# Optimization experiments

Measured on AMD Instinct MI355X. Metric: run time of the kernel, lower is better.

Reference implementation:

```python
import jax, jax.numpy as jnp
import numpy as np

H = 4      # num_heads
F = 64     # node_in_feats
FE = 16    # edge_in_feats
N = 4096   # num_nodes
E = 65536  # num_edges (avg degree 16)


def setup_inputs() -> dict:
    key = jax.random.key(0)
    ks = jax.random.split(key, 6)
    return {
        "node_inputs": jax.random.normal(ks[0], (N, F), jnp.float32),
        "edge_inputs": jax.random.normal(ks[1], (E, FE), jnp.float32),
        "src": jax.random.randint(ks[2], (E,), 0, N, jnp.int32),
        "dst": jax.random.randint(ks[3], (E,), 0, N, jnp.int32),
        "Wn": jax.random.normal(ks[4], (F, F * H), jnp.float32) / np.sqrt(F).astype(np.float32),
        "bn": jnp.zeros((F * H,), jnp.float32),
        "We": jax.random.normal(ks[5], (FE, H), jnp.float32) / np.sqrt(FE).astype(np.float32),
        "be": jnp.zeros((H,), jnp.float32),
    }


def reference(node_inputs, edge_inputs, src, dst, Wn, bn, We, be):
    # node linear projection: [N, H*F] then torch .view(H, -1, F) == row-major reshape
    node_proj = (node_inputs @ Wn + bn).reshape(H, N, F)
    # edge linear projection: [E, H] then torch .view(H, -1, 1) == row-major reshape
    edge_proj = (edge_inputs @ We + be).reshape(H, E)
    # self-attention: scale by sqrt(edge_in_feats), softmax over dim=1 (all edges per head)
    attn = jax.nn.softmax(edge_proj / np.float32(np.sqrt(FE)), axis=1)  # [H, E]
    # dense attention projection: projection[h, src[e], dst[e]] = attn[h, e]
    proj = jnp.zeros((H, N, N), jnp.float32).at[:, src, dst].set(attn)  # [H, N, N]
    # message passing ('sum' aggregation): proj @ node_proj -> [H, N, F]
    msg = jnp.einsum('hsd,hdf->hsf', proj, node_proj)
    # head pooling 'mean' over head dim (-3)
    return msg.mean(axis=0)  # [N, F]
```

## Files before the change

kernel.cpp:

```cpp
#include <hip/hip_runtime.h>

#define TBL_BITS 18
#define TBL_SIZE (1u << TBL_BITS)
#define TBL_MASK (TBL_SIZE - 1u)

#define GBLK 1024
#define BLK  256


struct Args {
    const float* X;  const float* Xe;
    const int* src;  const int* dst;
    const float* Wn; const float* bn;
    const float* We; const float* be;
    float* out;
    float* nproj;
    float* ep;
    float* partials;
    float* stats;
    unsigned long long* tbl;
};

__device__ __forceinline__ unsigned hash_key(unsigned key) {
    return (key * 2654435761u) >> (32 - TBL_BITS);
}

__global__ __launch_bounds__(BLK, 4) void k_p0(Args A) {
    const int tid = blockIdx.x * BLK + threadIdx.x;
    {
        const float4 z = make_float4(0.f, 0.f, 0.f, 0.f);
        if (tid < 65536)       ((float4*)A.out)[tid] = z;
        else if (tid < 196608) ((float4*)A.tbl)[tid - 65536] = z;
    }
    if (tid < 131072) {
        const int c = tid & 255;
        const int g = tid >> 8;
        const float b = A.bn[c];
        float acc[8];
#pragma unroll
        for (int r = 0; r < 8; ++r) acc[r] = b;
        const float* Wc = A.Wn + c;
#pragma unroll 8
        for (int k = 0; k < 64; ++k) {
            const float w = Wc[k * 256];
#pragma unroll
            for (int r = 0; r < 8; ++r)
                acc[r] = fmaf(A.X[(g + 512 * r) * 64 + k], w, acc[r]);
        }
#pragma unroll
        for (int r = 0; r < 8; ++r)
            A.nproj[(g + 512 * r) * 256 + c] = acc[r];
    }
    if (tid < 65536) {
        const float4* xi = (const float4*)(A.Xe + (size_t)tid * 16);
        float x[16];
        float4 v;
        v = xi[0]; x[0]=v.x;  x[1]=v.y;  x[2]=v.z;  x[3]=v.w;
        v = xi[1]; x[4]=v.x;  x[5]=v.y;  x[6]=v.z;  x[7]=v.w;
        v = xi[2]; x[8]=v.x;  x[9]=v.y;  x[10]=v.z; x[11]=v.w;
        v = xi[3]; x[12]=v.x; x[13]=v.y; x[14]=v.z; x[15]=v.w;
        float a0 = A.be[0], a1 = A.be[1], a2 = A.be[2], a3 = A.be[3];
#pragma unroll
        for (int k = 0; k < 16; ++k) {
            a0 = fmaf(x[k], A.We[k * 4 + 0], a0);
            a1 = fmaf(x[k], A.We[k * 4 + 1], a1);
            a2 = fmaf(x[k], A.We[k * 4 + 2], a2);
            a3 = fmaf(x[k], A.We[k * 4 + 3], a3);
        }
        const float e0 = expf(a0 * 0.25f), e1 = expf(a1 * 0.25f);
        const float e2 = expf(a2 * 0.25f), e3 = expf(a3 * 0.25f);
        ((float4*)A.ep)[tid] = make_float4(e0, e1, e2, e3);
        float s = e0 + e1 + e2 + e3;
#pragma unroll
        for (int off = 32; off > 0; off >>= 1) s += __shfl_xor(s, off);
        if ((tid & 63) == 0) A.partials[tid >> 6] = s;
    }
}

__global__ __launch_bounds__(BLK, 4) void k_p1(Args A) {
    const int tid = blockIdx.x * BLK + threadIdx.x;
    {
        const unsigned key = ((unsigned)A.src[tid] << 12) | (unsigned)A.dst[tid];
        const unsigned long long tag  = (unsigned long long)(key + 1u);
        const unsigned long long pack = (tag << 24) | (unsigned long long)tid;
        unsigned i = hash_key(key);
        while (true) {
            unsigned long long cur = A.tbl[i];
            if (cur == 0ull) {
                unsigned long long old = atomicCAS(&A.tbl[i], 0ull, pack);
                if (old == 0ull) break;
                cur = old;
            }
            if ((cur >> 24) == tag) {
                atomicMax(&A.tbl[i], pack);
                break;
            }
            i = (i + 1u) & TBL_MASK;
        }
    }
    if (blockIdx.x == 0) {
        __shared__ float4 red[256];
        const int t = threadIdx.x;
        red[t] = make_float4(A.partials[t], A.partials[256 + t],
                             A.partials[512 + t], A.partials[768 + t]);
        __syncthreads();
        for (int s = 128; s > 0; s >>= 1) {
            if (t < s) {
                red[t].x += red[t + s].x; red[t].y += red[t + s].y;
                red[t].z += red[t + s].z; red[t].w += red[t + s].w;
            }
            __syncthreads();
        }
        if (t == 0) {
            A.stats[0] = 0.25f / red[0].x;
            A.stats[1] = 0.25f / red[0].y;
            A.stats[2] = 0.25f / red[0].z;
            A.stats[3] = 0.25f / red[0].w;
        }
    }
}

__global__ __launch_bounds__(BLK, 4) void k_p2(Args A) {
    const int tid = blockIdx.x * BLK + threadIdx.x;
    const int w = tid >> 6;
    const int f = tid & 63;
    const float r0 = A.stats[0], r1 = A.stats[1];
    const float r2 = A.stats[2], r3 = A.stats[3];
#pragma unroll
    for (int i = 0; i < 8; i += 4) {
        int e[4], s[4], d[4];
        unsigned long long tag[4], cur[4];
        unsigned idx[4];
#pragma unroll
        for (int j = 0; j < 4; ++j) {
            e[j] = w * 8 + i + j;
            s[j] = A.src[e[j]];
            d[j] = A.dst[e[j]];
            const unsigned key = ((unsigned)s[j] << 12) | (unsigned)d[j];
            tag[j] = (unsigned long long)(key + 1u);
            idx[j] = hash_key(key);
        }
#pragma unroll
        for (int j = 0; j < 4; ++j) cur[j] = A.tbl[idx[j]];
#pragma unroll
        for (int j = 0; j < 4; ++j)
            while ((cur[j] >> 24) != tag[j]) {
                idx[j] = (idx[j] + 1u) & TBL_MASK;
                cur[j] = A.tbl[idx[j]];
            }
#pragma unroll
        for (int j = 0; j < 4; ++j) {
            if ((unsigned)(cur[j] & 0xFFFFFFull) != (unsigned)e[j]) continue;
            const float a0 = A.ep[e[j]];
            const float a1 = A.ep[65536 + e[j]];
            const float a2 = A.ep[131072 + e[j]];
            const float a3 = A.ep[196608 + e[j]];
            const int base = d[j] * 64 + f;
            float v = a0 * r0 * A.nproj[base];
            v = fmaf(a1 * r1, A.nproj[base + 262144], v);
            v = fmaf(a2 * r2, A.nproj[base + 524288], v);
            v = fmaf(a3 * r3, A.nproj[base + 786432], v);
            unsafeAtomicAdd(&A.out[s[j] * 64 + f], v);
        }
    }
}

extern "C" void kernel_launch(void* const* d_in, const int* in_sizes, int n_in,
                              void* d_out, int out_size, void* d_ws, size_t ws_size,
                              hipStream_t stream) {
    Args A;
    A.X   = (const float*)d_in[0];
    A.Xe  = (const float*)d_in[1];
    A.src = (const int*)d_in[2];
    A.dst = (const int*)d_in[3];
    A.Wn  = (const float*)d_in[4];
    A.bn  = (const float*)d_in[5];
    A.We  = (const float*)d_in[6];
    A.be  = (const float*)d_in[7];
    A.out = (float*)d_out;
    char* ws     = (char*)d_ws;
    A.nproj      = (float*)ws;
    A.ep         = (float*)(ws + 4u * 1024u * 1024u);
    A.partials   = (float*)(ws + 5u * 1024u * 1024u);
    A.stats      = (float*)(ws + 5u * 1024u * 1024u + 16384u);
    A.tbl        = (unsigned long long*)(ws + 6u * 1024u * 1024u);

    k_p0<<<GBLK, BLK, 0, stream>>>(A);
    k_p1<<<256, BLK, 0, stream>>>(A);
    k_p2<<<2048, BLK, 0, stream>>>(A);
}
```

Before: 52.56 us.

## Fuse hash dedup into scatter kernel with add-then-subtract correction for duplicates

Merges the hash-table insertion kernel and the scatter/aggregate kernel into one launch. Each block also recomputes the softmax normalisation redundantly in shared memory, so the separate stats buffer goes away. Duplicate (src,dst) edges are resolved on the fly: whichever edge wins the atomicMax adds its contribution and subtracts the contribution of the edge it displaced, so the last-index-wins semantics hold without a second lookup pass. This removes one launch and the global round-trip for the table, but it adds per-block redundant reduction work and extra atomic traffic, and its correctness relies on floating-point cancellation being exact enough.

```diff
diff --git a/kernel.cpp b/kernel.cpp
--- a/kernel.cpp
+++ b/kernel.cpp
@@ -17,7 +17,6 @@
     float* nproj;
     float* ep;
     float* partials;
-    float* stats;
     unsigned long long* tbl;
 };
 
@@ -25,7 +24,7 @@
     return (key * 2654435761u) >> (32 - TBL_BITS);
 }
 
-__global__ __launch_bounds__(BLK, 4) void k_p0(Args A) {
+__global__ __launch_bounds__(BLK, 4) void k_a(Args A) {
     const int tid = blockIdx.x * BLK + threadIdx.x;
     {
         const float4 z = make_float4(0.f, 0.f, 0.f, 0.f);
@@ -77,29 +76,10 @@
     }
 }
 
-__global__ __launch_bounds__(BLK, 4) void k_p1(Args A) {
-    const int tid = blockIdx.x * BLK + threadIdx.x;
+__global__ __launch_bounds__(BLK, 4) void k_b(Args A) {
+    __shared__ float4 red[256];
+    __shared__ float s_stats[4];
     {
-        const unsigned key = ((unsigned)A.src[tid] << 12) | (unsigned)A.dst[tid];
-        const unsigned long long tag  = (unsigned long long)(key + 1u);
-        const unsigned long long pack = (tag << 24) | (unsigned long long)tid;
-        unsigned i = hash_key(key);
-        while (true) {
-            unsigned long long cur = A.tbl[i];
-            if (cur == 0ull) {
-                unsigned long long old = atomicCAS(&A.tbl[i], 0ull, pack);
-                if (old == 0ull) break;
-                cur = old;
-            }
-            if ((cur >> 24) == tag) {
-                atomicMax(&A.tbl[i], pack);
-                break;
-            }
-            i = (i + 1u) & TBL_MASK;
-        }
-    }
-    if (blockIdx.x == 0) {
-        __shared__ float4 red[256];
         const int t = threadIdx.x;
         red[t] = make_float4(A.partials[t], A.partials[256 + t],
                              A.partials[512 + t], A.partials[768 + t]);
@@ -112,55 +92,73 @@
             __syncthreads();
         }
         if (t == 0) {
-            A.stats[0] = 0.25f / red[0].x;
-            A.stats[1] = 0.25f / red[0].y;
-            A.stats[2] = 0.25f / red[0].z;
-            A.stats[3] = 0.25f / red[0].w;
+            s_stats[0] = 0.25f / red[0].x;
+            s_stats[1] = 0.25f / red[0].y;
+            s_stats[2] = 0.25f / red[0].z;
+            s_stats[3] = 0.25f / red[0].w;
         }
+        __syncthreads();
     }
-}
+    const float r0 = s_stats[0], r1 = s_stats[1];
+    const float r2 = s_stats[2], r3 = s_stats[3];
 
-__global__ __launch_bounds__(BLK, 4) void k_p2(Args A) {
-    const int tid = blockIdx.x * BLK + threadIdx.x;
-    const int w = tid >> 6;
-    const int f = tid & 63;
-    const float r0 = A.stats[0], r1 = A.stats[1];
-    const float r2 = A.stats[2], r3 = A.stats[3];
+    const int tid  = blockIdx.x * BLK + threadIdx.x;
+    const int w    = tid >> 6;
+    const int lane = tid & 63;
+
 #pragma unroll
     for (int i = 0; i < 8; i += 4) {
-        int e[4], s[4], d[4];
-        unsigned long long tag[4], cur[4];
-        unsigned idx[4];
+        const int ebase = w * 8 + i;
+        int action = 0;
+        int sub_e  = -1;
+        if (lane < 4) {
+            const int e = ebase + lane;
+            const unsigned key = ((unsigned)A.src[e] << 12) | (unsigned)A.dst[e];
+            const unsigned long long tag  = (unsigned long long)(key + 1u);
+            const unsigned long long pack = (tag << 24) | (unsigned long long)e;
+            unsigned idx = hash_key(key);
+            while (true) {
+                unsigned long long cur = A.tbl[idx];
+                if (cur == 0ull) {
+                    unsigned long long old = atomicCAS(&A.tbl[idx], 0ull, pack);
+                    if (old == 0ull) { action = 1; break; }
+                    cur = old;
+                }
+                if ((cur >> 24) == tag) {
+                    const unsigned long long old = atomicMax(&A.tbl[idx], pack);
+                    if (old < pack) {
+                        action = 1;
+                        sub_e = (int)(old & 0xFFFFFFull);
+                    }
+                    break;
+                }
+                idx = (idx + 1u) & TBL_MASK;
+            }
+        }
 #pragma unroll
         for (int j = 0; j < 4; ++j) {
-            e[j] = w * 8 + i + j;
-            s[j] = A.src[e[j]];
-            d[j] = A.dst[e[j]];
-            const unsigned key = ((unsigned)s[j] << 12) | (unsigned)d[j];
-            tag[j] = (unsigned long long)(key + 1u);
-            idx[j] = hash_key(key);
-        }
-#pragma unroll
-        for (int j = 0; j < 4; ++j) cur[j] = A.tbl[idx[j]];
-#pragma unroll
-        for (int j = 0; j < 4; ++j)
-            while ((cur[j] >> 24) != tag[j]) {
-                idx[j] = (idx[j] + 1u) & TBL_MASK;
-                cur[j] = A.tbl[idx[j]];
+            const int act = __shfl(action, j);
+            if (!act) continue;
+            const int e  = ebase + j;
+            const int sj = A.src[e];
+            const int dj = A.dst[e];
+            const int se = __shfl(sub_e, j);
+            float c0 = A.ep[e];
+            float c1 = A.ep[65536 + e];
+            float c2 = A.ep[131072 + e];
+            float c3 = A.ep[196608 + e];
+            if (se >= 0) {
+                c0 -= A.ep[se];
+                c1 -= A.ep[65536 + se];
+                c2 -= A.ep[131072 + se];
+                c3 -= A.ep[196608 + se];
             }
-#pragma unroll
-        for (int j = 0; j < 4; ++j) {
-            if ((unsigned)(cur[j] & 0xFFFFFFull) != (unsigned)e[j]) continue;
-            const float a0 = A.ep[e[j]];
-            const float a1 = A.ep[65536 + e[j]];
-            const float a2 = A.ep[131072 + e[j]];
-            const float a3 = A.ep[196608 + e[j]];
-            const int base = d[j] * 64 + f;
-            float v = a0 * r0 * A.nproj[base];
-            v = fmaf(a1 * r1, A.nproj[base + 262144], v);
-            v = fmaf(a2 * r2, A.nproj[base + 524288], v);
-            v = fmaf(a3 * r3, A.nproj[base + 786432], v);
-            unsafeAtomicAdd(&A.out[s[j] * 64 + f], v);
+            const int base = dj * 64 + lane;
+            float v = c0 * r0 * A.nproj[base];
+            v = fmaf(c1 * r1, A.nproj[base + 262144], v);
+            v = fmaf(c2 * r2, A.nproj[base + 524288], v);
+            v = fmaf(c3 * r3, A.nproj[base + 786432], v);
+            unsafeAtomicAdd(&A.out[sj * 64 + lane], v);
         }
     }
 }
@@ -178,14 +176,12 @@
     A.We  = (const float*)d_in[6];
     A.be  = (const float*)d_in[7];
     A.out = (float*)d_out;
-    char* ws     = (char*)d_ws;
-    A.nproj      = (float*)ws;
-    A.ep         = (float*)(ws + 4u * 1024u * 1024u);
-    A.partials   = (float*)(ws + 5u * 1024u * 1024u);
-    A.stats      = (float*)(ws + 5u * 1024u * 1024u + 16384u);
-    A.tbl        = (unsigned long long*)(ws + 6u * 1024u * 1024u);
+    char* ws   = (char*)d_ws;
+    A.nproj    = (float*)ws;
+    A.ep       = (float*)(ws + 4u * 1024u * 1024u);
+    A.partials = (float*)(ws + 5u * 1024u * 1024u);
+    A.tbl      = (unsigned long long*)(ws + 6u * 1024u * 1024u);
 
-    k_p0<<<GBLK, BLK, 0, stream>>>(A);
-    k_p1<<<256, BLK, 0, stream>>>(A);
-    k_p2<<<2048, BLK, 0, stream>>>(A);
+    k_a<<<GBLK, BLK, 0, stream>>>(A);
+    k_b<<<2048, BLK, 0, stream>>>(A);
 }
```

Measured after the change: 46.42 us, median of 2. 1.13x faster.
